# Kernel optimization log

Measured on AMD Instinct MI355X. Metric: run time of the kernel, lower is better.

## Reference

```python
import jax, jax.numpy as jnp
import numpy as np

B, T, D = 4, 1024, 768
HW = 32            # H = W = sqrt(T)
DS = D // 16       # d_state = 48
CHUNK = 8          # items_each_chunk (must divide W)


def _ln(x, w, b, eps=1e-5):
    mu = x.mean(-1, keepdims=True)
    var = ((x - mu) ** 2).mean(-1, keepdims=True)
    return (x - mu) / jnp.sqrt(var + eps) * w + b


def _conv1x1(x, w):  # x: (B,C,H,W), w: (O,C)
    return jnp.einsum('bchw,oc->bohw', x, w)


def _dwconv(x, w, b, pad):  # depthwise conv, w: (C,1,k,k)
    y = jax.lax.conv_general_dilated(
        x, w, (1, 1), [(pad, pad), (pad, pad)],
        dimension_numbers=('NCHW', 'OIHW', 'NCHW'),
        feature_group_count=x.shape[1])
    if b is not None:
        y = y + b[None, :, None, None]
    return y


def _norm_gates(Gl, Gm, Gr):
    gl, gm, gr = jax.nn.sigmoid(Gl), jax.nn.sigmoid(Gm), jax.nn.sigmoid(Gr)
    s = gl + gm + gr
    s = s.at[:, :, 0, :].set(gm[:, :, 0, :] + gr[:, :, 0, :])    # top row: no h-1 neighbor
    s = s.at[:, :, -1, :].set(gl[:, :, -1, :] + gm[:, :, -1, :])  # bottom row: no h+1 neighbor
    s = jnp.maximum(s, 1e-7)
    return gl / s, gm / s, gr / s


def _gspn_scan(X, L, Gl, Gm, Gr, chunk):
    # GateRecurrent2dnoind: scan along W in independent chunks of `chunk` columns.
    # H[:, :, h, t] = L*X + Gl*Hprev[h-1] + Gm*Hprev[h] + Gr*Hprev[h+1], Hprev=0 at chunk start.
    b, c, h, w = X.shape
    nc = w // chunk

    def to_scan(a):  # (B,C,H,W) -> (chunk, B, C, H, nc)
        return a.reshape(b, c, h, nc, chunk).transpose(4, 0, 1, 2, 3)

    xs, ls, gls, gms, grs = map(to_scan, (X, L, Gl, Gm, Gr))

    def step(hprev, inp):
        x, l, gl, gm, gr = inp
        h_up = jnp.pad(hprev[:, :, :-1], ((0, 0), (0, 0), (1, 0), (0, 0)))
        h_dn = jnp.pad(hprev[:, :, 1:], ((0, 0), (0, 0), (0, 1), (0, 0)))
        hn = l * x + gl * h_up + gm * hprev + gr * h_dn
        return hn, hn

    _, ys = jax.lax.scan(step, jnp.zeros((b, c, h, nc), X.dtype), (xs, ls, gls, gms, grs))
    return ys.transpose(1, 2, 3, 4, 0).reshape(b, c, h, w)


def setup_inputs() -> dict:
    key = jax.random.key(0)
    ks = jax.random.split(key, 16)
    s = 0.02
    return {
        'hidden_states': jax.random.normal(ks[0], (B, T, D), jnp.float32),
        'norm_w': jnp.ones((D,), jnp.float32),
        'norm_b': jnp.zeros((D,), jnp.float32),
        'in_proj_w': jax.random.normal(ks[1], (D, D), jnp.float32) * s,
        'conv7_w': jax.random.normal(ks[2], (D, 1, 7, 7), jnp.float32) * s,
        'conv7_b': jnp.zeros((D,), jnp.float32),
        'xdown_w': jax.random.normal(ks[3], (DS, D), jnp.float32) * s,
        'wup_w': jax.random.normal(ks[4], (12 * D, DS), jnp.float32) * s,
        'lup_w': jax.random.normal(ks[5], (4 * D, DS), jnp.float32) * s,
        'uup_w': jax.random.normal(ks[6], (4 * D, DS), jnp.float32) * s,
        'dcoef_w': jax.random.normal(ks[7], (4 * D, DS), jnp.float32) * s,
        'm_w': jax.random.normal(ks[8], (4,), jnp.float32) * 0.25,
        'outconv_w': jax.random.normal(ks[9], (D, D), jnp.float32) * s,
        'outdconv_w': jax.random.normal(ks[10], (D, 1, 3, 3), jnp.float32) * s,
        'outproj_w': jax.random.normal(ks[11], (D, D), jnp.float32) * s,
    }


def reference(hidden_states, norm_w, norm_b, in_proj_w, conv7_w, conv7_b,
              xdown_w, wup_w, lup_w, uup_w, dcoef_w, m_w,
              outconv_w, outdconv_w, outproj_w):
    b, t, d = hidden_states.shape
    hh = ww = HW
    shortcut = hidden_states
    x = _ln(shortcut, norm_w, norm_b)                      # (B,T,D)
    x = x.transpose(0, 2, 1).reshape(b, d, hh, ww)         # (B,D,H,W)
    x = _conv1x1(x, in_proj_w)
    x = _dwconv(x, conv7_w, conv7_b, 3)
    xp = _conv1x1(x, xdown_w)                              # (B,ds,H,W)
    ws = _conv1x1(xp, wup_w)                               # (B,12D,H,W)
    Ls = _conv1x1(xp, lup_w)                               # (B,4D,H,W)
    Us = _conv1x1(xp, uup_w)
    Ds = _conv1x1(xp, dcoef_w)
    # 4 scan directions: [x, x^T, flip_w(x), flip_w(x^T)]
    x_hwwh = jnp.stack([x, x.transpose(0, 1, 3, 2)], axis=1)       # (B,2,D,H,W)
    xs = jnp.concatenate([x_hwwh, x_hwwh[..., ::-1]], axis=1)      # (B,4,D,H,W)
    xs = xs.reshape(b, 4 * d, hh, ww)
    Gl, Gm, Gr = ws[:, :4 * d], ws[:, 4 * d:8 * d], ws[:, 8 * d:]
    gl, gm, gr = _norm_gates(Gl, Gm, Gr)
    out = _gspn_scan(xs, Ls, gl, gm, gr, CHUNK)
    out = out * Us + xs * Ds
    out = out.reshape(b, 4, d, hh, ww)
    out = jnp.einsum('bkdhw,k->bdhw', out, m_w)            # m_conv (1x1 over 4 dirs)
    out = _conv1x1(out, outconv_w)
    out = _dwconv(out, outdconv_w, None, 1)
    out = out * jax.nn.relu(out)
    out = out.reshape(b, d, t).transpose(0, 2, 1)
    out = out @ outproj_w.T
    return out, shortcut
```

## Files before the change

### kernel.cpp

```cpp
#include <hip/hip_runtime.h>

typedef unsigned short u16;
typedef unsigned int u32;
typedef __attribute__((ext_vector_type(8))) short short8v;
typedef __attribute__((ext_vector_type(4))) float f32x4;
typedef __attribute__((ext_vector_type(2))) unsigned u32x2v;

#define DD 768
#define PP 1024
#define NTOK 4096

__device__ __forceinline__ u16 f2bf(float f) {
  u32 u = __builtin_bit_cast(u32, f);
  u += 0x7fffu + ((u >> 16) & 1u);
  return (u16)(u >> 16);
}
__device__ __forceinline__ float b2f(u16 v) {
  return __builtin_bit_cast(float, (u32)v << 16);
}
__device__ __forceinline__ u32 pk_trunc(float fa, float fb) {
  return __builtin_amdgcn_perm(__builtin_bit_cast(u32, fa), __builtin_bit_cast(u32, fb), 0x07060302u);
}
__device__ __forceinline__ float ex8(const short8v& v, int j) {
  const u32 dw = ((const u32*)&v)[j >> 1];
  return __builtin_bit_cast(float, (j & 1) ? (dw & 0xffff0000u) : (dw << 16));
}

__global__ __launch_bounds__(256) void prep_ln_k(const float* __restrict__ hs,
                                                 const float* __restrict__ gw, const float* __restrict__ gb,
                                                 u16* __restrict__ lnout, float* __restrict__ shortcut,
                                                 const float* __restrict__ win, u16* __restrict__ wInB,
                                                 const float* __restrict__ wout, u16* __restrict__ wOutB,
                                                 const float* __restrict__ wprj, u16* __restrict__ wPrjB,
                                                 const float* __restrict__ xdw, u16* __restrict__ wXdB,
                                                 const float* __restrict__ wup, const float* __restrict__ lup,
                                                 const float* __restrict__ uup, const float* __restrict__ dco,
                                                 u16* __restrict__ wB) {
  const int id = blockIdx.x;
  const int t = threadIdx.x;
  if (id < 4096) {
    const int tok = id;
    const float* xr = hs + (size_t)tok * DD;
    float v0 = xr[t], v1 = xr[t + 256], v2 = xr[t + 512];
    float s = v0 + v1 + v2;
    float q = v0 * v0 + v1 * v1 + v2 * v2;
#pragma unroll
    for (int off = 32; off > 0; off >>= 1) {
      s += __shfl_down(s, off, 64);
      q += __shfl_down(q, off, 64);
    }
    __shared__ float ss[4], qs[4];
    const int wid = t >> 6, lane = t & 63;
    if (lane == 0) { ss[wid] = s; qs[wid] = q; }
    __syncthreads();
    const float st = ss[0] + ss[1] + ss[2] + ss[3];
    const float qt = qs[0] + qs[1] + qs[2] + qs[3];
    const float mu = st * (1.f / 768.f);
    const float var = qt * (1.f / 768.f) - mu * mu;
    const float rstd = rsqrtf(var + 1e-5f);
    float* sc = shortcut + (size_t)tok * DD;
    u16* lo = lnout + (size_t)tok * DD;
    sc[t] = v0; sc[t + 256] = v1; sc[t + 512] = v2;
    lo[t]       = f2bf((v0 - mu) * rstd * gw[t] + gb[t]);
    lo[t + 256] = f2bf((v1 - mu) * rstd * gw[t + 256] + gb[t + 256]);
    lo[t + 512] = f2bf((v2 - mu) * rstd * gw[t + 512] + gb[t + 512]);
    return;
  }
  const int id2 = id - 4096;
  if (id2 < 6912) {
    const int m = id2 / 2304;
    const int i = (id2 - m * 2304) * 256 + t;
    const float* s = (m == 0) ? win : (m == 1) ? wout : wprj;
    u16* d = (m == 0) ? wInB : (m == 1) ? wOutB : wPrjB;
    d[i] = f2bf(s[i]);
  } else if (id2 < 7104) {
    const int i = (id2 - 6912) * 256 + t;
    const int r = i / DD;
    wXdB[i] = (r < 48) ? f2bf(xdw[i]) : (u16)0;
  } else {
    const int c = id2 - 7104;
    u16* dst = wB + (size_t)c * 2048;
    for (int i = t; i < 2048; i += 256) {
      const int row = i >> 6, s = i & 63;
      u16 v = 0;
      if (row < 24 && s < 48) {
        const int k = row & 3, type = row >> 2;
        const int ch = k * DD + c;
        const float* src;
        if (type < 3) src = wup + ((size_t)(type * 3072 + ch)) * 48;
        else if (type == 3) src = lup + (size_t)ch * 48;
        else if (type == 4) src = uup + (size_t)ch * 48;
        else src = dco + (size_t)ch * 48;
        v = f2bf(src[s]);
      }
      dst[i] = v;
    }
  }
}

template <int BSRC>
__global__ __launch_bounds__(256) void gemm_bf16(const u16* __restrict__ A,
                                                 const u16* __restrict__ Bt,
                                                 void* __restrict__ outv, const int mode) {
  __shared__ u16 Al[64][40];
  __shared__ u16 BlF[144 * 40];
  const int t = threadIdx.x;
  const int ntile = blockIdx.x * 128;
  const int mtile = blockIdx.y * 64;
  const int bb = ntile >> 10, pq0 = ntile & 1023;
  const int wid = t >> 6, lane = t & 63;
  const int m0 = (wid & 1) * 32, n0 = (wid >> 1) * 64;
  const int l15 = lane & 15, quad = lane >> 4;
  f32x4 acc[2][4];
#pragma unroll
  for (int mi = 0; mi < 2; ++mi)
#pragma unroll
    for (int ni = 0; ni < 4; ++ni) acc[mi][ni] = (f32x4){0.f, 0.f, 0.f, 0.f};
  const int ra = t >> 2, sa = t & 3;
  const u16* ag = A + (size_t)(mtile + ra) * DD + sa * 8;
  const int rb = t >> 1, hb = t & 1;
  const u16* bg = Bt + (size_t)(ntile + rb) * DD + hb * 16;
  const int chp = t >> 4, tokg = t & 15, tok0 = tokg * 8;
  const u16* bgc = Bt + ((size_t)(bb * DD + chp * 2)) * PP + pq0 + tok0;
  for (int k0 = 0; k0 < DD; k0 += 32) {
    const uint4 av = *reinterpret_cast<const uint4*>(ag + k0);
    uint4 bv0, bv1;
    if (BSRC == 0) {
      bv0 = *reinterpret_cast<const uint4*>(bg + k0);
      bv1 = *reinterpret_cast<const uint4*>(bg + k0 + 8);
    } else {
      bv0 = *reinterpret_cast<const uint4*>(bgc + (size_t)k0 * PP);
      bv1 = *reinterpret_cast<const uint4*>(bgc + (size_t)(k0 + 1) * PP);
    }
    __syncthreads();
    *reinterpret_cast<uint4*>(&Al[ra][sa * 8]) = av;
    if (BSRC == 0) {
      const int pr = rb + (rb >> 3);
      *reinterpret_cast<uint4*>(&BlF[pr * 40 + hb * 16]) = bv0;
      *reinterpret_cast<uint4*>(&BlF[pr * 40 + hb * 16 + 8]) = bv1;
    } else {
      union { uint4 v; u16 u[8]; } ua, ub;
      ua.v = bv0; ub.v = bv1;
#pragma unroll
      for (int i2 = 0; i2 < 8; ++i2) {
        const int tk = tok0 + i2;
        *reinterpret_cast<u32*>(&BlF[(tk + (tk >> 3)) * 40 + chp * 2]) =
            (u32)ua.u[i2] | ((u32)ub.u[i2] << 16);
      }
    }
    __syncthreads();
    short8v af[2];
#pragma unroll
    for (int mi = 0; mi < 2; ++mi)
      af[mi] = *reinterpret_cast<const short8v*>(&Al[m0 + mi * 16 + l15][quad * 8]);
    short8v bfr[4];
#pragma unroll
    for (int ni = 0; ni < 4; ++ni) {
      const int tl = n0 + ni * 16 + l15;
      bfr[ni] = *reinterpret_cast<const short8v*>(&BlF[(tl + (tl >> 3)) * 40 + quad * 8]);
    }
#pragma unroll
    for (int mi = 0; mi < 2; ++mi)
#pragma unroll
      for (int ni = 0; ni < 4; ++ni)
        acc[mi][ni] = __builtin_amdgcn_mfma_f32_16x16x32_bf16(af[mi], bfr[ni], acc[mi][ni], 0, 0, 0);
  }
#pragma unroll
  for (int mi = 0; mi < 2; ++mi) {
#pragma unroll
    for (int ni = 0; ni < 4; ++ni) {
      const int ob = mtile + m0 + mi * 16 + quad * 4;
      const int pg = ntile + n0 + ni * 16 + l15;
      if (mode == 1) {
        *reinterpret_cast<f32x4*>((float*)outv + (size_t)pg * DD + ob) = acc[mi][ni];
      } else {
        const int pq = pg & 1023;
        u16* dstb = (u16*)outv;
#pragma unroll
        for (int r = 0; r < 4; ++r)
          dstb[((size_t)(bb * DD + ob + r)) * PP + pq] = f2bf(acc[mi][ni][r]);
      }
    }
  }
}

__global__ __launch_bounds__(256) void xdgemm_k(const u16* __restrict__ A,
                                                const u16* __restrict__ Ycm,
                                                u16* __restrict__ xpA) {
  __shared__ u16 Al[64][72];
  __shared__ u16 Bl[16][72];
  const int t = threadIdx.x;
  const int ntile = blockIdx.x * 16;
  const int bb = ntile >> 10, pq0 = ntile & 1023;
  const int wid = t >> 6, lane = t & 63, l15 = lane & 15, quad = lane >> 4;
  f32x4 acc = (f32x4){0.f, 0.f, 0.f, 0.f};
  const int arow = t >> 2, aks = (t & 3) * 16;
  const u16* ag = A + (size_t)arow * DD + aks;
  const int chp = t >> 3;
  const int tk0 = (t & 7) * 2;
  const u16* bg0 = Ycm + ((size_t)(bb * DD + chp * 2)) * PP + pq0 + tk0;
  for (int k0 = 0; k0 < DD; k0 += 64) {
    const uint4 a0 = *reinterpret_cast<const uint4*>(ag + k0);
    const uint4 a1 = *reinterpret_cast<const uint4*>(ag + k0 + 8);
    const u32 b0 = *reinterpret_cast<const u32*>(bg0 + (size_t)k0 * PP);
    const u32 b1 = *reinterpret_cast<const u32*>(bg0 + (size_t)(k0 + 1) * PP);
    __syncthreads();
    *reinterpret_cast<uint4*>(&Al[arow][aks]) = a0;
    *reinterpret_cast<uint4*>(&Al[arow][aks + 8]) = a1;
    *reinterpret_cast<u32*>(&Bl[tk0][chp * 2]) = (b0 & 0xffffu) | (b1 << 16);
    *reinterpret_cast<u32*>(&Bl[tk0 + 1][chp * 2]) = (b0 >> 16) | (b1 & 0xffff0000u);
    __syncthreads();
#pragma unroll
    for (int ks = 0; ks < 2; ++ks) {
      const short8v af = *reinterpret_cast<const short8v*>(&Al[wid * 16 + l15][ks * 32 + quad * 8]);
      const short8v bf = *reinterpret_cast<const short8v*>(&Bl[l15][ks * 32 + quad * 8]);
      acc = __builtin_amdgcn_mfma_f32_16x16x32_bf16(af, bf, acc, 0, 0, 0);
    }
  }
  const int pq = pq0 + l15;
  const int i = ((pq & 31) >> 4) * 512 + (pq >> 5) * 16 + (pq & 15);
  u16* dst = xpA + ((size_t)(bb * 1024 + i)) * 64 + wid * 16 + quad * 4;
  *reinterpret_cast<uint2*>(dst) = make_uint2(pk_trunc(acc[1], acc[0]), pk_trunc(acc[3], acc[2]));
}

__global__ __launch_bounds__(256) void dwconv7_k(const u16* __restrict__ x,
                                                 const float* __restrict__ wgt,
                                                 const float* __restrict__ bias,
                                                 u16* __restrict__ y) {
  const int bc = blockIdx.x;
  const int c = bc % DD;
  __shared__ float tile[38 * 38];
  __shared__ float wl[49];
  __shared__ float bsh[1];
  const int t = threadIdx.x;
  for (int i = t; i < 38 * 38; i += 256) tile[i] = 0.f;
  __syncthreads();
  const u16* xr = x + (size_t)bc * PP;
  for (int i = t; i < 512; i += 256) {
    const u32 v = reinterpret_cast<const u32*>(xr)[i];
    const int p0 = i * 2;
    const int h = p0 >> 5, w = p0 & 31;
    tile[(h + 3) * 38 + w + 3] = b2f((u16)v);
    tile[(h + 3) * 38 + w + 4] = b2f((u16)(v >> 16));
  }
  if (t < 49) wl[t] = wgt[c * 49 + t];
  if (t == 0) bsh[0] = bias[c];
  __syncthreads();
  u16* yo = y + (size_t)bc * PP;
  const int w = t & 31, hb = t >> 5;
  const float bv = bsh[0];
  float a0 = bv, a1 = bv, a2 = bv, a3 = bv;
#pragma unroll
  for (int rr = 0; rr < 10; ++rr) {
    float row[7];
#pragma unroll
    for (int kw = 0; kw < 7; ++kw) row[kw] = tile[(hb * 4 + rr) * 38 + w + kw];
    if (rr < 7) {
#pragma unroll
      for (int kw = 0; kw < 7; ++kw) a0 = fmaf(wl[rr * 7 + kw], row[kw], a0);
    }
    if (rr >= 1 && rr < 8) {
#pragma unroll
      for (int kw = 0; kw < 7; ++kw) a1 = fmaf(wl[(rr - 1) * 7 + kw], row[kw], a1);
    }
    if (rr >= 2 && rr < 9) {
#pragma unroll
      for (int kw = 0; kw < 7; ++kw) a2 = fmaf(wl[(rr - 2) * 7 + kw], row[kw], a2);
    }
    if (rr >= 3) {
#pragma unroll
      for (int kw = 0; kw < 7; ++kw) a3 = fmaf(wl[(rr - 3) * 7 + kw], row[kw], a3);
    }
  }
  yo[(hb * 4 + 0) * 32 + w] = f2bf(a0);
  yo[(hb * 4 + 1) * 32 + w] = f2bf(a1);
  yo[(hb * 4 + 2) * 32 + w] = f2bf(a2);
  yo[(hb * 4 + 3) * 32 + w] = f2bf(a3);
}

__global__ __launch_bounds__(256) void dwconv3_k(const u16* __restrict__ x,
                                                 const float* __restrict__ wgt,
                                                 u16* __restrict__ y) {
  const int bc = blockIdx.x;
  const int c = bc % DD;
  __shared__ float tile[34 * 34];
  __shared__ float wl[9];
  const int t = threadIdx.x;
  for (int i = t; i < 34 * 34; i += 256) tile[i] = 0.f;
  __syncthreads();
  const u16* xr = x + (size_t)bc * PP;
  for (int i = t; i < 512; i += 256) {
    const u32 v = reinterpret_cast<const u32*>(xr)[i];
    const int p0 = i * 2;
    const int h = p0 >> 5, w = p0 & 31;
    tile[(h + 1) * 34 + w + 1] = b2f((u16)v);
    tile[(h + 1) * 34 + w + 2] = b2f((u16)(v >> 16));
  }
  if (t < 9) wl[t] = wgt[c * 9 + t];
  __syncthreads();
  u16* yo = y + (size_t)bc * PP;
  const int w = t & 31, hb = t >> 5;
  float a0 = 0.f, a1 = 0.f, a2 = 0.f, a3 = 0.f;
#pragma unroll
  for (int rr = 0; rr < 6; ++rr) {
    float row[3];
#pragma unroll
    for (int kw = 0; kw < 3; ++kw) row[kw] = tile[(hb * 4 + rr) * 34 + w + kw];
    if (rr < 3) {
#pragma unroll
      for (int kw = 0; kw < 3; ++kw) a0 = fmaf(wl[rr * 3 + kw], row[kw], a0);
    }
    if (rr >= 1 && rr < 4) {
#pragma unroll
      for (int kw = 0; kw < 3; ++kw) a1 = fmaf(wl[(rr - 1) * 3 + kw], row[kw], a1);
    }
    if (rr >= 2 && rr < 5) {
#pragma unroll
      for (int kw = 0; kw < 3; ++kw) a2 = fmaf(wl[(rr - 2) * 3 + kw], row[kw], a2);
    }
    if (rr >= 3) {
#pragma unroll
      for (int kw = 0; kw < 3; ++kw) a3 = fmaf(wl[(rr - 3) * 3 + kw], row[kw], a3);
    }
  }
  const float r0 = a0 > 0.f ? a0 * a0 : 0.f;
  const float r1 = a1 > 0.f ? a1 * a1 : 0.f;
  const float r2 = a2 > 0.f ? a2 * a2 : 0.f;
  const float r3 = a3 > 0.f ? a3 * a3 : 0.f;
  yo[(hb * 4 + 0) * 32 + w] = f2bf(r0);
  yo[(hb * 4 + 1) * 32 + w] = f2bf(r1);
  yo[(hb * 4 + 2) * 32 + w] = f2bf(r2);
  yo[(hb * 4 + 3) * 32 + w] = f2bf(r3);
}

#define ACT_SWZ(row, col) ((col) ^ (((((col) >> 6) ^ (row)) & 7) << 3))
#define PSWZ(r) ((((r) ^ ((r) >> 3)) & 3) << 3)

__device__ __forceinline__ void produce_half(u16* __restrict__ actbuf,
                                             const u16* __restrict__ ab,
                                             const short8v bw[2][2],
                                             int l15, int quad, int g) {
#pragma unroll
  for (int mt = 0; mt < 8; ++mt) {
    const u16* ar = ab + (mt * 16 + l15) * 64 + quad * 8;
    const short8v a0 = *reinterpret_cast<const short8v*>(ar);
    const short8v a1 = *reinterpret_cast<const short8v*>(ar + 32);
    f32x4 acc0 = {0.f, 0.f, 0.f, 0.f}, acc1 = {0.f, 0.f, 0.f, 0.f};
    acc0 = __builtin_amdgcn_mfma_f32_16x16x32_bf16(a0, bw[0][0], acc0, 0, 0, 0);
    acc0 = __builtin_amdgcn_mfma_f32_16x16x32_bf16(a1, bw[0][1], acc0, 0, 0, 0);
    acc1 = __builtin_amdgcn_mfma_f32_16x16x32_bf16(a0, bw[1][0], acc1, 0, 0, 0);
    acc1 = __builtin_amdgcn_mfma_f32_16x16x32_bf16(a1, bw[1][1], acc1, 0, 0, 0);
    const int qb = g * 128 + mt * 16 + quad * 4;
    const int cs = ACT_SWZ(l15, qb);
    *reinterpret_cast<uint2*>(&actbuf[l15 * 512 + cs]) =
        make_uint2(pk_trunc(acc0[1], acc0[0]), pk_trunc(acc0[3], acc0[2]));
    if (l15 < 8)
      *reinterpret_cast<uint2*>(&actbuf[(16 + l15) * 512 + cs]) =
          make_uint2(pk_trunc(acc1[1], acc1[0]), pk_trunc(acc1[3], acc1[2]));
  }
}

__device__ __forceinline__ void consume_half(const u16* __restrict__ actbuf,
                                             const u16* __restrict__ planeTc,
                                             const u16* __restrict__ y2row,
                                             u16* __restrict__ outpc,
                                             float mw, int dpair, int cs2, int d, int h, int half) {
  const int k = dpair * 2 + d;
  const int hc = half * 2 + cs2;
  const int colb = h * 16 + cs2 * 8;
  const int wst = dpair ? (24 - hc * 8) : (hc * 8);
  short8v vPr;
  if (d == 0) vPr = *reinterpret_cast<const short8v*>(y2row + h * 32 + wst);
  else        vPr = *reinterpret_cast<const short8v*>(planeTc + h * 40 + (wst ^ PSWZ(h)));
  short8v vPe;
  {
    const u32* s = (const u32*)&vPr;
    u32* dq = (u32*)&vPe;
    if (dpair) {
      dq[0] = (s[3] >> 16) | (s[3] << 16);
      dq[1] = (s[2] >> 16) | (s[2] << 16);
      dq[2] = (s[1] >> 16) | (s[1] << 16);
      dq[3] = (s[0] >> 16) | (s[0] << 16);
    } else {
      dq[0] = s[0]; dq[1] = s[1]; dq[2] = s[2]; dq[3] = s[3];
    }
  }
#define ACTP(row) (*reinterpret_cast<const short8v*>(&actbuf[(row) * 512 + ACT_SWZ((row), colb)]))
  const short8v vGl = ACTP(0 + k);
  const short8v vGm = ACTP(4 + k);
  const short8v vGr = ACTP(8 + k);
  const short8v vL  = ACTP(12 + k);
  const short8v vU  = ACTP(16 + k);
  const short8v vD  = ACTP(20 + k);
#undef ACTP
  const bool top = (h == 0), bot = (h == 31);
  float H = 0.f, prev = 0.f;
  u32 ox[4];
#pragma unroll
  for (int j = 0; j < 8; ++j) {
    float el = __expf(-ex8(vGl, j));
    const float em = __expf(-ex8(vGm, j));
    float er = __expf(-ex8(vGr, j));
    if (top) el = 1e30f;
    if (bot) er = 1e30f;
    const float pl2 = 1.f + el, pm = 1.f + em, pr = 1.f + er;
    const float ul = pm * pr, um = pl2 * pr, ur = pl2 * pm;
    const float rcpS = __builtin_amdgcn_rcpf(ul + um + ur);
    const float xv = ex8(vPe, j);
    const float Lx = ex8(vL, j) * xv;
    const int Hb = __builtin_bit_cast(int, H);
    const float up = __builtin_bit_cast(float,
        __builtin_amdgcn_update_dpp(0, Hb, 0x138, 0xf, 0xf, true));
    const float dn = __builtin_bit_cast(float,
        __builtin_amdgcn_update_dpp(0, Hb, 0x130, 0xf, 0xf, true));
    H = fmaf(ul * rcpS, up, fmaf(um * rcpS, H, fmaf(ur * rcpS, dn, Lx)));
    float part = fmaf(H, ex8(vU, j), xv * ex8(vD, j)) * mw;
#if __has_builtin(__builtin_amdgcn_permlane32_swap)
    u32x2v sw = __builtin_amdgcn_permlane32_swap(__builtin_bit_cast(u32, part),
                                                 __builtin_bit_cast(u32, part), false, false);
    part = __builtin_bit_cast(float, sw[0]) + __builtin_bit_cast(float, sw[1]);
#else
    part += __shfl_xor(part, 32, 64);
#endif
    if (j & 1) ox[j >> 1] = pk_trunc(part, prev);
    else prev = part;
  }
  if (d == 0) {
    uint4 o;
    o.x = ox[0]; o.y = ox[1]; o.z = ox[2]; o.w = ox[3];
    *reinterpret_cast<uint4*>(&outpc[h * 64 + dpair * 32 + ((hc * 8) ^ ((h & 3) << 3))]) = o;
  }
}

__global__ __launch_bounds__(512, 4) void scan_k(const u16* __restrict__ y2b,
                                                 const u16* __restrict__ xpA,
                                                 const u16* __restrict__ wB,
                                                 const float* __restrict__ mwp,
                                                 u16* __restrict__ out1) {
  const int bc2 = blockIdx.x;
  const int b = bc2 / 384;
  const int cpair = bc2 - b * 384;
  const int c0 = cpair * 2;
  __shared__ __align__(16) u16 actA[24 * 512];
  __shared__ __align__(16) u16 actB[24 * 512];
  __shared__ __align__(16) u16 planeT[2][1280];
  __shared__ __align__(16) u16 outp[2][32 * 64];
  const int t = threadIdx.x;
  const int wid = t >> 6, lane = t & 63, l15 = lane & 15, quad = lane >> 4;
  const int ch = wid >> 2;
  const int g = wid & 3;
  const int dpair = g & 1, cs2 = g >> 1;
  const int d = lane >> 5, h = lane & 31;
  const int c = c0 + ch;
  const int bc = b * DD + c;
  {
    const int pch = t >> 8, idx = t & 255;
    const u16* yp = y2b + (size_t)(b * DD + c0 + pch) * PP;
#pragma unroll
    for (int i2 = 0; i2 < 2; ++i2) {
      const int i = idx + i2 * 256;
      const u32 v = reinterpret_cast<const u32*>(yp)[i];
      const int p0 = i * 2;
      const int hh = p0 >> 5, ww = p0 & 31;
      planeT[pch][ww * 40 + (hh ^ PSWZ(ww))] = (u16)v;
      planeT[pch][(ww + 1) * 40 + (hh ^ PSWZ(ww + 1))] = (u16)(v >> 16);
    }
  }
  const u16* wc = wB + (size_t)c * 2048;
  short8v bw[2][2];
#pragma unroll
  for (int nt = 0; nt < 2; ++nt)
#pragma unroll
    for (int ks = 0; ks < 2; ++ks)
      bw[nt][ks] = *reinterpret_cast<const short8v*>(wc + (nt * 16 + l15) * 64 + ks * 32 + quad * 8);
  const u16* xb = xpA + ((size_t)(b * 1024)) * 64;
  const u16* y2row = y2b + (size_t)bc * PP;
  const float mw = mwp[dpair * 2 + d];
  if (ch == 0) produce_half(actA, xb + (size_t)(g * 128) * 64, bw, l15, quad, g);
  __syncthreads();
  if (ch == 0) consume_half(actA, planeT[0], y2row, outp[0], mw, dpair, cs2, d, h, 0);
  else         produce_half(actB, xb + (size_t)(g * 128) * 64, bw, l15, quad, g);
  __syncthreads();
  if (ch == 1) consume_half(actB, planeT[1], y2row, outp[1], mw, dpair, cs2, d, h, 0);
  else         produce_half(actA, xb + (size_t)(512 + g * 128) * 64, bw, l15, quad, g);
  __syncthreads();
  if (ch == 0) consume_half(actA, planeT[0], y2row, outp[0], mw, dpair, cs2, d, h, 1);
  else         produce_half(actB, xb + (size_t)(512 + g * 128) * 64, bw, l15, quad, g);
  __syncthreads();
  if (ch == 1) consume_half(actB, planeT[1], y2row, outp[1], mw, dpair, cs2, d, h, 1);
  __syncthreads();
  const int hh2 = t >> 4, wp = t & 15;
  const int wsw = (wp * 2) ^ ((hh2 & 3) << 3);
#pragma unroll
  for (int cc = 0; cc < 2; ++cc) {
    const u32 u0 = *reinterpret_cast<const u32*>(&outp[cc][hh2 * 64 + wsw]);
    const u32 u1 = *reinterpret_cast<const u32*>(&outp[cc][hh2 * 64 + 32 + wsw]);
    const float v0 = b2f((u16)u0) + b2f((u16)u1);
    const float v1 = b2f((u16)(u0 >> 16)) + b2f((u16)(u1 >> 16));
    *reinterpret_cast<u32*>(out1 + (size_t)(b * DD + c0 + cc) * PP + hh2 * 32 + wp * 2) =
        pk_trunc(v1, v0);
  }
}

extern "C" void kernel_launch(void* const* d_in, const int* in_sizes, int n_in,
                              void* d_out, int out_size, void* d_ws, size_t ws_size,
                              hipStream_t stream) {
  const float* hs   = (const float*)d_in[0];
  const float* nw   = (const float*)d_in[1];
  const float* nb   = (const float*)d_in[2];
  const float* win  = (const float*)d_in[3];
  const float* c7w  = (const float*)d_in[4];
  const float* c7b  = (const float*)d_in[5];
  const float* xdw  = (const float*)d_in[6];
  const float* wupw = (const float*)d_in[7];
  const float* lupw = (const float*)d_in[8];
  const float* uupw = (const float*)d_in[9];
  const float* dcow = (const float*)d_in[10];
  const float* mww  = (const float*)d_in[11];
  const float* wout = (const float*)d_in[12];
  const float* odw  = (const float*)d_in[13];
  const float* wprj = (const float*)d_in[14];
  float* out0 = (float*)d_out;
  float* shortcut = out0 + (size_t)NTOK * DD;

  char* ws = (char*)d_ws;
  u16* lnA    = (u16*)(ws + 0);
  u16* wInB   = (u16*)(ws + 6291456);
  u16* wOutB  = (u16*)(ws + 7471104);
  u16* wPrjB  = (u16*)(ws + 8650752);
  u16* wB     = (u16*)(ws + 9830400);
  u16* wXdB   = (u16*)(ws + 12976128);
  u16* xpA    = (u16*)(ws + 13074432);
  u16* y1b    = (u16*)(ws + 13598720);
  u16* y2b    = (u16*)(ws + 19890176);
  u16* out1   = (u16*)(ws + 26181632);
  u16* y3b    = y1b;
  u16* y4b    = out1;

  prep_ln_k<<<11968, 256, 0, stream>>>(hs, nw, nb, lnA, shortcut,
                                       win, wInB, wout, wOutB, wprj, wPrjB,
                                       xdw, wXdB, wupw, lupw, uupw, dcow, wB);
  gemm_bf16<0><<<dim3(32, 12), 256, 0, stream>>>(wInB, lnA, y1b, 3);
  dwconv7_k<<<3072, 256, 0, stream>>>(y1b, c7w, c7b, y2b);
  xdgemm_k<<<256, 256, 0, stream>>>(wXdB, y2b, xpA);
  scan_k<<<1536, 512, 0, stream>>>(y2b, xpA, wB, mww, out1);
  gemm_bf16<1><<<dim3(32, 12), 256, 0, stream>>>(wOutB, out1, y3b, 3);
  dwconv3_k<<<3072, 256, 0, stream>>>(y3b, odw, y4b);
  gemm_bf16<1><<<dim3(32, 12), 256, 0, stream>>>(wPrjB, y4b, out0, 1);
}
```

Baseline: 232.7 us.

## Split scan block into dedicated producer and consumer warps with two-chain scans

Warps are now assigned fixed roles: four warps do all the MFMA gate production for both channels, and four warps do the scans, each handling two independent column chunks interleaved in one loop. Interleaving the two recurrence chains is meant to hide DPP, exp and rcp latency through ILP. Fixed roles also keep per-channel weights resident in the producer warps. In exchange, only two of the four consumer warps are active in each phase, so scan parallelism per phase halves, and consumer register pressure rises.

```diff
diff --git a/kernel.cpp b/kernel.cpp
--- a/kernel.cpp
+++ b/kernel.cpp
@@ -24,6 +24,23 @@
 __device__ __forceinline__ float ex8(const short8v& v, int j) {
   const u32 dw = ((const u32*)&v)[j >> 1];
   return __builtin_bit_cast(float, (j & 1) ? (dw & 0xffff0000u) : (dw << 16));
+}
+__device__ __forceinline__ float dpp_shr1(float x) {
+  return __builtin_bit_cast(float,
+      __builtin_amdgcn_update_dpp(0, __builtin_bit_cast(int, x), 0x138, 0xf, 0xf, true));
+}
+__device__ __forceinline__ float dpp_shl1(float x) {
+  return __builtin_bit_cast(float,
+      __builtin_amdgcn_update_dpp(0, __builtin_bit_cast(int, x), 0x130, 0xf, 0xf, true));
+}
+__device__ __forceinline__ float xhalf_sum(float p) {
+#if __has_builtin(__builtin_amdgcn_permlane32_swap)
+  u32x2v sw = __builtin_amdgcn_permlane32_swap(__builtin_bit_cast(u32, p),
+                                               __builtin_bit_cast(u32, p), false, false);
+  return __builtin_bit_cast(float, sw[0]) + __builtin_bit_cast(float, sw[1]);
+#else
+  return p + __shfl_xor(p, 32, 64);
+#endif
 }
 
 __global__ __launch_bounds__(256) void prep_ln_k(const float* __restrict__ hs,
@@ -360,75 +377,93 @@
   }
 }
 
-__device__ __forceinline__ void consume_half(const u16* __restrict__ actbuf,
-                                             const u16* __restrict__ planeTc,
-                                             const u16* __restrict__ y2row,
-                                             u16* __restrict__ outpc,
-                                             float mw, int dpair, int cs2, int d, int h, int half) {
+__device__ __forceinline__ void consume2(const u16* __restrict__ actbuf,
+                                         const u16* __restrict__ planeTc,
+                                         const u16* __restrict__ y2row,
+                                         u16* __restrict__ outpc,
+                                         float mw, int dpair, int d, int h, int half) {
   const int k = dpair * 2 + d;
-  const int hc = half * 2 + cs2;
-  const int colb = h * 16 + cs2 * 8;
-  const int wst = dpair ? (24 - hc * 8) : (hc * 8);
-  short8v vPr;
-  if (d == 0) vPr = *reinterpret_cast<const short8v*>(y2row + h * 32 + wst);
-  else        vPr = *reinterpret_cast<const short8v*>(planeTc + h * 40 + (wst ^ PSWZ(h)));
-  short8v vPe;
+  const int hc0 = half * 2, hc1 = hc0 + 1;
+  const int wst0 = dpair ? (24 - hc0 * 8) : (hc0 * 8);
+  const int wst1 = dpair ? (24 - hc1 * 8) : (hc1 * 8);
+  short8v vPr0, vPr1;
+  if (d == 0) {
+    vPr0 = *reinterpret_cast<const short8v*>(y2row + h * 32 + wst0);
+    vPr1 = *reinterpret_cast<const short8v*>(y2row + h * 32 + wst1);
+  } else {
+    vPr0 = *reinterpret_cast<const short8v*>(planeTc + h * 40 + (wst0 ^ PSWZ(h)));
+    vPr1 = *reinterpret_cast<const short8v*>(planeTc + h * 40 + (wst1 ^ PSWZ(h)));
+  }
+  short8v vP0, vP1;
   {
-    const u32* s = (const u32*)&vPr;
-    u32* dq = (u32*)&vPe;
+    const u32* s0 = (const u32*)&vPr0; u32* q0 = (u32*)&vP0;
+    const u32* s1 = (const u32*)&vPr1; u32* q1 = (u32*)&vP1;
     if (dpair) {
-      dq[0] = (s[3] >> 16) | (s[3] << 16);
-      dq[1] = (s[2] >> 16) | (s[2] << 16);
-      dq[2] = (s[1] >> 16) | (s[1] << 16);
-      dq[3] = (s[0] >> 16) | (s[0] << 16);
+      q0[0] = (s0[3] >> 16) | (s0[3] << 16); q0[1] = (s0[2] >> 16) | (s0[2] << 16);
+      q0[2] = (s0[1] >> 16) | (s0[1] << 16); q0[3] = (s0[0] >> 16) | (s0[0] << 16);
+      q1[0] = (s1[3] >> 16) | (s1[3] << 16); q1[1] = (s1[2] >> 16) | (s1[2] << 16);
+      q1[2] = (s1[1] >> 16) | (s1[1] << 16); q1[3] = (s1[0] >> 16) | (s1[0] << 16);
     } else {
-      dq[0] = s[0]; dq[1] = s[1]; dq[2] = s[2]; dq[3] = s[3];
-    }
-  }
-#define ACTP(row) (*reinterpret_cast<const short8v*>(&actbuf[(row) * 512 + ACT_SWZ((row), colb)]))
-  const short8v vGl = ACTP(0 + k);
-  const short8v vGm = ACTP(4 + k);
-  const short8v vGr = ACTP(8 + k);
-  const short8v vL  = ACTP(12 + k);
-  const short8v vU  = ACTP(16 + k);
-  const short8v vD  = ACTP(20 + k);
-#undef ACTP
+      q0[0] = s0[0]; q0[1] = s0[1]; q0[2] = s0[2]; q0[3] = s0[3];
+      q1[0] = s1[0]; q1[1] = s1[1]; q1[2] = s1[2]; q1[3] = s1[3];
+    }
+  }
+  const int colb0 = h * 16, colb1 = h * 16 + 8;
+  const u16* bA0 = actbuf + k * 512 + ACT_SWZ(k, colb0);
+  const u16* bB0 = actbuf + (4 + k) * 512 + ACT_SWZ(4 + k, colb0);
+  const u16* bA1 = actbuf + k * 512 + ACT_SWZ(k, colb1);
+  const u16* bB1 = actbuf + (4 + k) * 512 + ACT_SWZ(4 + k, colb1);
+  const short8v vGl0 = *reinterpret_cast<const short8v*>(bA0);
+  const short8v vGm0 = *reinterpret_cast<const short8v*>(bB0);
+  const short8v vGr0 = *reinterpret_cast<const short8v*>(bA0 + 8 * 512);
+  const short8v vL0  = *reinterpret_cast<const short8v*>(bB0 + 8 * 512);
+  const short8v vU0  = *reinterpret_cast<const short8v*>(bA0 + 16 * 512);
+  const short8v vD0  = *reinterpret_cast<const short8v*>(bB0 + 16 * 512);
+  const short8v vGl1 = *reinterpret_cast<const short8v*>(bA1);
+  const short8v vGm1 = *reinterpret_cast<const short8v*>(bB1);
+  const short8v vGr1 = *reinterpret_cast<const short8v*>(bA1 + 8 * 512);
+  const short8v vL1  = *reinterpret_cast<const short8v*>(bB1 + 8 * 512);
+  const short8v vU1  = *reinterpret_cast<const short8v*>(bA1 + 16 * 512);
+  const short8v vD1  = *reinterpret_cast<const short8v*>(bB1 + 16 * 512);
   const bool top = (h == 0), bot = (h == 31);
-  float H = 0.f, prev = 0.f;
-  u32 ox[4];
+  float H0 = 0.f, H1 = 0.f, pv0 = 0.f, pv1 = 0.f;
+  u32 ox0[4], ox1[4];
 #pragma unroll
   for (int j = 0; j < 8; ++j) {
-    float el = __expf(-ex8(vGl, j));
-    const float em = __expf(-ex8(vGm, j));
-    float er = __expf(-ex8(vGr, j));
-    if (top) el = 1e30f;
-    if (bot) er = 1e30f;
-    const float pl2 = 1.f + el, pm = 1.f + em, pr = 1.f + er;
-    const float ul = pm * pr, um = pl2 * pr, ur = pl2 * pm;
-    const float rcpS = __builtin_amdgcn_rcpf(ul + um + ur);
-    const float xv = ex8(vPe, j);
-    const float Lx = ex8(vL, j) * xv;
-    const int Hb = __builtin_bit_cast(int, H);
-    const float up = __builtin_bit_cast(float,
-        __builtin_amdgcn_update_dpp(0, Hb, 0x138, 0xf, 0xf, true));
-    const float dn = __builtin_bit_cast(float,
-        __builtin_amdgcn_update_dpp(0, Hb, 0x130, 0xf, 0xf, true));
-    H = fmaf(ul * rcpS, up, fmaf(um * rcpS, H, fmaf(ur * rcpS, dn, Lx)));
-    float part = fmaf(H, ex8(vU, j), xv * ex8(vD, j)) * mw;
-#if __has_builtin(__builtin_amdgcn_permlane32_swap)
-    u32x2v sw = __builtin_amdgcn_permlane32_swap(__builtin_bit_cast(u32, part),
-                                                 __builtin_bit_cast(u32, part), false, false);
-    part = __builtin_bit_cast(float, sw[0]) + __builtin_bit_cast(float, sw[1]);
-#else
-    part += __shfl_xor(part, 32, 64);
-#endif
-    if (j & 1) ox[j >> 1] = pk_trunc(part, prev);
-    else prev = part;
+    float el0 = __expf(-ex8(vGl0, j));
+    const float em0 = __expf(-ex8(vGm0, j));
+    float er0 = __expf(-ex8(vGr0, j));
+    float el1 = __expf(-ex8(vGl1, j));
+    const float em1 = __expf(-ex8(vGm1, j));
+    float er1 = __expf(-ex8(vGr1, j));
+    if (top) { el0 = 1e30f; el1 = 1e30f; }
+    if (bot) { er0 = 1e30f; er1 = 1e30f; }
+    const float pl0 = 1.f + el0, pm0 = 1.f + em0, pr0 = 1.f + er0;
+    const float pl1 = 1.f + el1, pm1 = 1.f + em1, pr1 = 1.f + er1;
+    const float ul0 = pm0 * pr0, um0 = pl0 * pr0, ur0 = pl0 * pm0;
+    const float ul1 = pm1 * pr1, um1 = pl1 * pr1, ur1 = pl1 * pm1;
+    const float rs0 = __builtin_amdgcn_rcpf(ul0 + um0 + ur0);
+    const float rs1 = __builtin_amdgcn_rcpf(ul1 + um1 + ur1);
+    const float xv0 = ex8(vP0, j), xv1 = ex8(vP1, j);
+    const float Lx0 = ex8(vL0, j) * xv0, Lx1 = ex8(vL1, j) * xv1;
+    const float up0 = dpp_shr1(H0), dn0 = dpp_shl1(H0);
+    const float up1 = dpp_shr1(H1), dn1 = dpp_shl1(H1);
+    H0 = fmaf(ul0 * rs0, up0, fmaf(um0 * rs0, H0, fmaf(ur0 * rs0, dn0, Lx0)));
+    H1 = fmaf(ul1 * rs1, up1, fmaf(um1 * rs1, H1, fmaf(ur1 * rs1, dn1, Lx1)));
+    float p0 = fmaf(H0, ex8(vU0, j), xv0 * ex8(vD0, j)) * mw;
+    float p1 = fmaf(H1, ex8(vU1, j), xv1 * ex8(vD1, j)) * mw;
+    p0 = xhalf_sum(p0);
+    p1 = xhalf_sum(p1);
+    if (j & 1) { ox0[j >> 1] = pk_trunc(p0, pv0); ox1[j >> 1] = pk_trunc(p1, pv1); }
+    else { pv0 = p0; pv1 = p1; }
   }
   if (d == 0) {
-    uint4 o;
-    o.x = ox[0]; o.y = ox[1]; o.z = ox[2]; o.w = ox[3];
-    *reinterpret_cast<uint4*>(&outpc[h * 64 + dpair * 32 + ((hc * 8) ^ ((h & 3) << 3))]) = o;
+    uint4 o0, o1;
+    o0.x = ox0[0]; o0.y = ox0[1]; o0.z = ox0[2]; o0.w = ox0[3];
+    o1.x = ox1[0]; o1.y = ox1[1]; o1.z = ox1[2]; o1.w = ox1[3];
+    const int basew = h * 64 + dpair * 32;
+    *reinterpret_cast<uint4*>(&outpc[basew + ((hc0 * 8) ^ ((h & 3) << 3))]) = o0;
+    *reinterpret_cast<uint4*>(&outpc[basew + ((hc1 * 8) ^ ((h & 3) << 3))]) = o1;
   }
 }
 
@@ -447,12 +482,11 @@
   __shared__ __align__(16) u16 outp[2][32 * 64];
   const int t = threadIdx.x;
   const int wid = t >> 6, lane = t & 63, l15 = lane & 15, quad = lane >> 4;
-  const int ch = wid >> 2;
+  const int role = wid >> 2;
   const int g = wid & 3;
-  const int dpair = g & 1, cs2 = g >> 1;
+  const int cch = (wid >> 1) & 1;
+  const int dpair = wid & 1;
   const int d = lane >> 5, h = lane & 31;
-  const int c = c0 + ch;
-  const int bc = b * DD + c;
   {
     const int pch = t >> 8, idx = t & 255;
     const u16* yp = y2b + (size_t)(b * DD + c0 + pch) * PP;
@@ -466,28 +500,42 @@
       planeT[pch][(ww + 1) * 40 + (hh ^ PSWZ(ww + 1))] = (u16)(v >> 16);
     }
   }
-  const u16* wc = wB + (size_t)c * 2048;
-  short8v bw[2][2];
-#pragma unroll
-  for (int nt = 0; nt < 2; ++nt)
-#pragma unroll
-    for (int ks = 0; ks < 2; ++ks)
-      bw[nt][ks] = *reinterpret_cast<const short8v*>(wc + (nt * 16 + l15) * 64 + ks * 32 + quad * 8);
   const u16* xb = xpA + ((size_t)(b * 1024)) * 64;
-  const u16* y2row = y2b + (size_t)bc * PP;
+  short8v bw0[2][2], bw1[2][2];
+  if (role == 1) {
+    const u16* wc0p = wB + (size_t)c0 * 2048;
+    const u16* wc1p = wB + (size_t)(c0 + 1) * 2048;
+#pragma unroll
+    for (int nt = 0; nt < 2; ++nt)
+#pragma unroll
+      for (int ks = 0; ks < 2; ++ks) {
+        bw0[nt][ks] = *reinterpret_cast<const short8v*>(wc0p + (nt * 16 + l15) * 64 + ks * 32 + quad * 8);
+        bw1[nt][ks] = *reinterpret_cast<const short8v*>(wc1p + (nt * 16 + l15) * 64 + ks * 32 + quad * 8);
+      }
+    produce_half(actA, xb + (size_t)(g * 128) * 64, bw0, l15, quad, g);
+  }
+  const u16* y2row = y2b + (size_t)(b * DD + c0 + cch) * PP;
   const float mw = mwp[dpair * 2 + d];
-  if (ch == 0) produce_half(actA, xb + (size_t)(g * 128) * 64, bw, l15, quad, g);
-  __syncthreads();
-  if (ch == 0) consume_half(actA, planeT[0], y2row, outp[0], mw, dpair, cs2, d, h, 0);
-  else         produce_half(actB, xb + (size_t)(g * 128) * 64, bw, l15, quad, g);
-  __syncthreads();
-  if (ch == 1) consume_half(actB, planeT[1], y2row, outp[1], mw, dpair, cs2, d, h, 0);
-  else         produce_half(actA, xb + (size_t)(512 + g * 128) * 64, bw, l15, quad, g);
-  __syncthreads();
-  if (ch == 0) consume_half(actA, planeT[0], y2row, outp[0], mw, dpair, cs2, d, h, 1);
-  else         produce_half(actB, xb + (size_t)(512 + g * 128) * 64, bw, l15, quad, g);
-  __syncthreads();
-  if (ch == 1) consume_half(actB, planeT[1], y2row, outp[1], mw, dpair, cs2, d, h, 1);
+  __syncthreads();
+  if (role == 0) {
+    if (cch == 0) consume2(actA, planeT[0], y2row, outp[0], mw, dpair, d, h, 0);
+  } else {
+    produce_half(actB, xb + (size_t)(g * 128) * 64, bw1, l15, quad, g);
+  }
+  __syncthreads();
+  if (role == 0) {
+    if (cch == 1) consume2(actB, planeT[1], y2row, outp[1], mw, dpair, d, h, 0);
+  } else {
+    produce_half(actA, xb + (size_t)(512 + g * 128) * 64, bw0, l15, quad, g);
+  }
+  __syncthreads();
+  if (role == 0) {
+    if (cch == 0) consume2(actA, planeT[0], y2row, outp[0], mw, dpair, d, h, 1);
+  } else {
+    produce_half(actB, xb + (size_t)(512 + g * 128) * 64, bw1, l15, quad, g);
+  }
+  __syncthreads();
+  if (role == 0 && cch == 1) consume2(actB, planeT[1], y2row, outp[1], mw, dpair, d, h, 1);
   __syncthreads();
   const int hh2 = t >> 4, wp = t & 15;
   const int wsw = (wp * 2) ^ ((hh2 & 3) << 3);
```

New measurement: 235.0 us. No clear change (+1.0%).

## Double K-step to 64 with register prefetch in GEMM, raise scan wave priority

Applied to the files above, without the earlier changes.

The bf16 GEMM now processes K in steps of 64 instead of 32, halving the number of barrier pairs, and it prefetches the next K slice's global loads into registers while the current slice's MFMAs run. LDS tiles are widened to a 72-element stride to hold the larger slice. The scan consume routine raises wave priority with s_setprio around its serial recurrence so it is favoured over co-resident waves. DPP and cross-half reduction code is factored into helpers with no speed intent. The prefetch costs extra registers and more LDS per block, which may reduce occupancy.

```diff
diff --git a/kernel.cpp b/kernel.cpp
--- a/kernel.cpp
+++ b/kernel.cpp
@@ -24,6 +24,23 @@
 __device__ __forceinline__ float ex8(const short8v& v, int j) {
   const u32 dw = ((const u32*)&v)[j >> 1];
   return __builtin_bit_cast(float, (j & 1) ? (dw & 0xffff0000u) : (dw << 16));
+}
+__device__ __forceinline__ float dpp_shr1(float x) {
+  return __builtin_bit_cast(float,
+      __builtin_amdgcn_update_dpp(0, __builtin_bit_cast(int, x), 0x138, 0xf, 0xf, true));
+}
+__device__ __forceinline__ float dpp_shl1(float x) {
+  return __builtin_bit_cast(float,
+      __builtin_amdgcn_update_dpp(0, __builtin_bit_cast(int, x), 0x130, 0xf, 0xf, true));
+}
+__device__ __forceinline__ float xhalf_sum(float p) {
+#if __has_builtin(__builtin_amdgcn_permlane32_swap)
+  u32x2v sw = __builtin_amdgcn_permlane32_swap(__builtin_bit_cast(u32, p),
+                                               __builtin_bit_cast(u32, p), false, false);
+  return __builtin_bit_cast(float, sw[0]) + __builtin_bit_cast(float, sw[1]);
+#else
+  return p + __shfl_xor(p, 32, 64);
+#endif
 }
 
 __global__ __launch_bounds__(256) void prep_ln_k(const float* __restrict__ hs,
@@ -102,8 +119,8 @@
 __global__ __launch_bounds__(256) void gemm_bf16(const u16* __restrict__ A,
                                                  const u16* __restrict__ Bt,
                                                  void* __restrict__ outv, const int mode) {
-  __shared__ u16 Al[64][40];
-  __shared__ u16 BlF[144 * 40];
+  __shared__ u16 Al[64][72];
+  __shared__ u16 BlF[144 * 72];
   const int t = threadIdx.x;
   const int ntile = blockIdx.x * 128;
   const int mtile = blockIdx.y * 64;
@@ -117,54 +134,77 @@
 #pragma unroll
     for (int ni = 0; ni < 4; ++ni) acc[mi][ni] = (f32x4){0.f, 0.f, 0.f, 0.f};
   const int ra = t >> 2, sa = t & 3;
-  const u16* ag = A + (size_t)(mtile + ra) * DD + sa * 8;
+  const u16* ag = A + (size_t)(mtile + ra) * DD + sa * 16;
   const int rb = t >> 1, hb = t & 1;
-  const u16* bg = Bt + (size_t)(ntile + rb) * DD + hb * 16;
-  const int chp = t >> 4, tokg = t & 15, tok0 = tokg * 8;
-  const u16* bgc = Bt + ((size_t)(bb * DD + chp * 2)) * PP + pq0 + tok0;
-  for (int k0 = 0; k0 < DD; k0 += 32) {
-    const uint4 av = *reinterpret_cast<const uint4*>(ag + k0);
-    uint4 bv0, bv1;
-    if (BSRC == 0) {
-      bv0 = *reinterpret_cast<const uint4*>(bg + k0);
-      bv1 = *reinterpret_cast<const uint4*>(bg + k0 + 8);
-    } else {
-      bv0 = *reinterpret_cast<const uint4*>(bgc + (size_t)k0 * PP);
-      bv1 = *reinterpret_cast<const uint4*>(bgc + (size_t)(k0 + 1) * PP);
-    }
+  const u16* bg = Bt + (size_t)(ntile + rb) * DD + hb * 32;
+  const int chp = t >> 4, tok0 = (t & 15) * 8;
+  const u16* bgc0 = Bt + ((size_t)(bb * DD + chp * 2)) * PP + pq0 + tok0;
+  const u16* bgc1 = Bt + ((size_t)(bb * DD + (chp + 16) * 2)) * PP + pq0 + tok0;
+  uint4 pa0, pa1, pb0, pb1, pb2, pb3;
+#define LOADK(k0)                                                              \
+  {                                                                            \
+    pa0 = *reinterpret_cast<const uint4*>(ag + (k0));                          \
+    pa1 = *reinterpret_cast<const uint4*>(ag + (k0) + 8);                      \
+    if (BSRC == 0) {                                                           \
+      pb0 = *reinterpret_cast<const uint4*>(bg + (k0));                        \
+      pb1 = *reinterpret_cast<const uint4*>(bg + (k0) + 8);                    \
+      pb2 = *reinterpret_cast<const uint4*>(bg + (k0) + 16);                   \
+      pb3 = *reinterpret_cast<const uint4*>(bg + (k0) + 24);                   \
+    } else {                                                                   \
+      pb0 = *reinterpret_cast<const uint4*>(bgc0 + (size_t)(k0) * PP);         \
+      pb1 = *reinterpret_cast<const uint4*>(bgc0 + (size_t)((k0) + 1) * PP);   \
+      pb2 = *reinterpret_cast<const uint4*>(bgc1 + (size_t)(k0) * PP);         \
+      pb3 = *reinterpret_cast<const uint4*>(bgc1 + (size_t)((k0) + 1) * PP);   \
+    }                                                                          \
+  }
+  LOADK(0);
+  for (int k0 = 0; k0 < DD; k0 += 64) {
     __syncthreads();
-    *reinterpret_cast<uint4*>(&Al[ra][sa * 8]) = av;
+    *reinterpret_cast<uint4*>(&Al[ra][sa * 16]) = pa0;
+    *reinterpret_cast<uint4*>(&Al[ra][sa * 16 + 8]) = pa1;
     if (BSRC == 0) {
       const int pr = rb + (rb >> 3);
-      *reinterpret_cast<uint4*>(&BlF[pr * 40 + hb * 16]) = bv0;
-      *reinterpret_cast<uint4*>(&BlF[pr * 40 + hb * 16 + 8]) = bv1;
+      *reinterpret_cast<uint4*>(&BlF[pr * 72 + hb * 32]) = pb0;
+      *reinterpret_cast<uint4*>(&BlF[pr * 72 + hb * 32 + 8]) = pb1;
+      *reinterpret_cast<uint4*>(&BlF[pr * 72 + hb * 32 + 16]) = pb2;
+      *reinterpret_cast<uint4*>(&BlF[pr * 72 + hb * 32 + 24]) = pb3;
     } else {
-      union { uint4 v; u16 u[8]; } ua, ub;
-      ua.v = bv0; ub.v = bv1;
+      union { uint4 v; u16 u[8]; } ua, ub, uc, ud;
+      ua.v = pb0; ub.v = pb1; uc.v = pb2; ud.v = pb3;
 #pragma unroll
       for (int i2 = 0; i2 < 8; ++i2) {
-        const int tk = tok0 + i2;
-        *reinterpret_cast<u32*>(&BlF[(tk + (tk >> 3)) * 40 + chp * 2]) =
+        const int prow = (tok0 + i2 + ((tok0 + i2) >> 3)) * 72;
+        *reinterpret_cast<u32*>(&BlF[prow + chp * 2]) =
             (u32)ua.u[i2] | ((u32)ub.u[i2] << 16);
+        *reinterpret_cast<u32*>(&BlF[prow + chp * 2 + 32]) =
+            (u32)uc.u[i2] | ((u32)ud.u[i2] << 16);
       }
     }
     __syncthreads();
-    short8v af[2];
+    if (k0 + 64 < DD) LOADK(k0 + 64);
+    short8v af[2][2], bfr[4][2];
 #pragma unroll
     for (int mi = 0; mi < 2; ++mi)
-      af[mi] = *reinterpret_cast<const short8v*>(&Al[m0 + mi * 16 + l15][quad * 8]);
-    short8v bfr[4];
+#pragma unroll
+      for (int ks = 0; ks < 2; ++ks)
+        af[mi][ks] = *reinterpret_cast<const short8v*>(&Al[m0 + mi * 16 + l15][ks * 32 + quad * 8]);
 #pragma unroll
     for (int ni = 0; ni < 4; ++ni) {
       const int tl = n0 + ni * 16 + l15;
-      bfr[ni] = *reinterpret_cast<const short8v*>(&BlF[(tl + (tl >> 3)) * 40 + quad * 8]);
+      const int prow = (tl + (tl >> 3)) * 72;
+#pragma unroll
+      for (int ks = 0; ks < 2; ++ks)
+        bfr[ni][ks] = *reinterpret_cast<const short8v*>(&BlF[prow + ks * 32 + quad * 8]);
     }
 #pragma unroll
     for (int mi = 0; mi < 2; ++mi)
 #pragma unroll
-      for (int ni = 0; ni < 4; ++ni)
-        acc[mi][ni] = __builtin_amdgcn_mfma_f32_16x16x32_bf16(af[mi], bfr[ni], acc[mi][ni], 0, 0, 0);
-  }
+      for (int ni = 0; ni < 4; ++ni) {
+        acc[mi][ni] = __builtin_amdgcn_mfma_f32_16x16x32_bf16(af[mi][0], bfr[ni][0], acc[mi][ni], 0, 0, 0);
+        acc[mi][ni] = __builtin_amdgcn_mfma_f32_16x16x32_bf16(af[mi][1], bfr[ni][1], acc[mi][ni], 0, 0, 0);
+      }
+  }
+#undef LOADK
 #pragma unroll
   for (int mi = 0; mi < 2; ++mi) {
 #pragma unroll
@@ -365,6 +405,7 @@
                                              const u16* __restrict__ y2row,
                                              u16* __restrict__ outpc,
                                              float mw, int dpair, int cs2, int d, int h, int half) {
+  __builtin_amdgcn_s_setprio(1);
   const int k = dpair * 2 + d;
   const int hc = half * 2 + cs2;
   const int colb = h * 16 + cs2 * 8;
@@ -408,20 +449,11 @@
     const float rcpS = __builtin_amdgcn_rcpf(ul + um + ur);
     const float xv = ex8(vPe, j);
     const float Lx = ex8(vL, j) * xv;
-    const int Hb = __builtin_bit_cast(int, H);
-    const float up = __builtin_bit_cast(float,
-        __builtin_amdgcn_update_dpp(0, Hb, 0x138, 0xf, 0xf, true));
-    const float dn = __builtin_bit_cast(float,
-        __builtin_amdgcn_update_dpp(0, Hb, 0x130, 0xf, 0xf, true));
+    const float up = dpp_shr1(H);
+    const float dn = dpp_shl1(H);
     H = fmaf(ul * rcpS, up, fmaf(um * rcpS, H, fmaf(ur * rcpS, dn, Lx)));
     float part = fmaf(H, ex8(vU, j), xv * ex8(vD, j)) * mw;
-#if __has_builtin(__builtin_amdgcn_permlane32_swap)
-    u32x2v sw = __builtin_amdgcn_permlane32_swap(__builtin_bit_cast(u32, part),
-                                                 __builtin_bit_cast(u32, part), false, false);
-    part = __builtin_bit_cast(float, sw[0]) + __builtin_bit_cast(float, sw[1]);
-#else
-    part += __shfl_xor(part, 32, 64);
-#endif
+    part = xhalf_sum(part);
     if (j & 1) ox[j >> 1] = pk_trunc(part, prev);
     else prev = part;
   }
@@ -430,6 +462,7 @@
     o.x = ox[0]; o.y = ox[1]; o.z = ox[2]; o.w = ox[3];
     *reinterpret_cast<uint4*>(&outpc[h * 64 + dpair * 32 + ((hc * 8) ^ ((h & 3) << 3))]) = o;
   }
+  __builtin_amdgcn_s_setprio(0);
 }
 
 __global__ __launch_bounds__(512, 4) void scan_k(const u16* __restrict__ y2b,
```

After: 226.5 us. 1.03x faster.
